# Optimization experiments

Hardware: AMD Instinct MI355X
Metric: run time of the kernel (lower is better)

## Reference

```python
import jax, jax.numpy as jnp
import numpy as np

N = 50000          # nodes
E = 1_600_000      # edges
IN_DIM = 64
HID = 64
HEADS = 2
EDGE_DIM = 8
OUT_DIM = 2
NEG_SLOPE = 0.2    # PyG GATConv default negative_slope


def _gat_params(key, in_ch, out_ch, heads, edge_dim, concat):
    ks = jax.random.split(key, 6)
    s = 0.1
    W = jax.random.normal(ks[0], (in_ch, heads * out_ch), jnp.float32) * s
    a_src = jax.random.normal(ks[1], (heads, out_ch), jnp.float32) * s
    a_dst = jax.random.normal(ks[2], (heads, out_ch), jnp.float32) * s
    We = jax.random.normal(ks[3], (edge_dim, heads * out_ch), jnp.float32) * s
    a_e = jax.random.normal(ks[4], (heads, out_ch), jnp.float32) * s
    b = jnp.zeros((heads * out_ch if concat else out_ch,), jnp.float32)
    return W, a_src, a_dst, We, a_e, b


def gat_conv(x, edge_index, edge_attr, W, a_src, a_dst, We, a_e, b, heads, out_ch, concat):
    # Faithful PyG GATConv with edge_dim, add_self_loops=True, fill_value='mean'.
    n = x.shape[0]
    src0, dst0 = edge_index[0], edge_index[1]
    # self-loop edge_attr = mean of incoming edge attrs (scatter-mean over dst)
    cnt = jax.ops.segment_sum(jnp.ones((src0.shape[0],), x.dtype), dst0, num_segments=n)
    loop_attr = jax.ops.segment_sum(edge_attr, dst0, num_segments=n) / jnp.maximum(cnt, 1.0)[:, None]
    loop = jnp.arange(n, dtype=src0.dtype)
    src = jnp.concatenate([src0, loop])
    dst = jnp.concatenate([dst0, loop])
    ea = jnp.concatenate([edge_attr, loop_attr], axis=0)          # [E+N, edge_dim]

    h = (x @ W).reshape(n, heads, out_ch)                          # [N, H, C]
    al_src = jnp.einsum('nhc,hc->nh', h, a_src)                    # [N, H]
    al_dst = jnp.einsum('nhc,hc->nh', h, a_dst)
    e = (ea @ We).reshape(-1, heads, out_ch)                       # [E+N, H, C]
    al_edge = jnp.einsum('ehc,hc->eh', e, a_e)

    alpha = jax.nn.leaky_relu(al_src[src] + al_dst[dst] + al_edge, NEG_SLOPE)  # [E+N, H]
    # segment softmax over destination node (every dst has a self loop)
    amax = jax.ops.segment_max(alpha, dst, num_segments=n)
    ex = jnp.exp(alpha - amax[dst])
    denom = jax.ops.segment_sum(ex, dst, num_segments=n)
    w = ex / (denom[dst] + 1e-16)

    out = jax.ops.segment_sum(h[src] * w[:, :, None], dst, num_segments=n)     # [N, H, C]
    out = out.reshape(n, heads * out_ch) if concat else out.mean(axis=1)
    return out + b


def setup_inputs() -> dict:
    key = jax.random.key(0)
    ks = jax.random.split(key, 8)
    inp = {
        'x': jax.random.normal(ks[0], (N, IN_DIM), jnp.float32),
        'edge_index': jax.random.randint(ks[1], (2, E), 0, N, dtype=jnp.int32),
        'edge_attr': jax.random.normal(ks[2], (E, EDGE_DIM), jnp.float32),
    }
    # layer 0: in -> hid, heads=1, concat=True
    for name, p in zip(['W0', 'as0', 'ad0', 'We0', 'ae0', 'b0'], _gat_params(ks[3], IN_DIM, HID, 1, EDGE_DIM, True)):
        inp[name] = p
    # layers 1,2: hid -> hid, heads=HEADS, concat=False
    for name, p in zip(['W1', 'as1', 'ad1', 'We1', 'ae1', 'b1'], _gat_params(ks[4], HID, HID, HEADS, EDGE_DIM, False)):
        inp[name] = p
    for name, p in zip(['W2', 'as2', 'ad2', 'We2', 'ae2', 'b2'], _gat_params(ks[5], HID, HID, HEADS, EDGE_DIM, False)):
        inp[name] = p
    # final: hid -> out_dim, heads=1, concat=True
    for name, p in zip(['W3', 'as3', 'ad3', 'We3', 'ae3', 'b3'], _gat_params(ks[6], HID, OUT_DIM, 1, EDGE_DIM, True)):
        inp[name] = p
    return inp


def reference(x, edge_index, edge_attr,
              W0, as0, ad0, We0, ae0, b0,
              W1, as1, ad1, We1, ae1, b1,
              W2, as2, ad2, We2, ae2, b2,
              W3, as3, ad3, We3, ae3, b3):
    h = jax.nn.relu(gat_conv(x, edge_index, edge_attr, W0, as0, ad0, We0, ae0, b0, 1, HID, True))
    h = jax.nn.relu(gat_conv(h, edge_index, edge_attr, W1, as1, ad1, We1, ae1, b1, HEADS, HID, False))
    h = jax.nn.relu(gat_conv(h, edge_index, edge_attr, W2, as2, ad2, We2, ae2, b2, HEADS, HID, False))
    return gat_conv(h, edge_index, edge_attr, W3, as3, ad3, We3, ae3, b3, 1, OUT_DIM, True)
```

## Files before the change

### kernel.cpp

```cpp
#include <hip/hip_runtime.h>
#include <math.h>


#define GSZ 256
#define CAPB 10240
#define CHUNK 4096
#define CAP_C 9984

__device__ __forceinline__ float wave_sum64(float v) {
#pragma unroll
  for (int o = 32; o >= 1; o >>= 1) v += __shfl_xor(v, o);
  return v;
}
__device__ __forceinline__ float dot8(const float4& a, const float4& b,
                                      const float* c) {
  return a.x * c[0] + a.y * c[1] + a.z * c[2] + a.w * c[3] + b.x * c[4] +
         b.y * c[5] + b.z * c[6] + b.w * c[7];
}


__global__ __launch_bounds__(256) void bin_kernel(const int* __restrict__ src,
                                                  const int* __restrict__ dst,
                                                  int* __restrict__ bfill,
                                                  int2* __restrict__ bbuf,
                                                  int E_) {
  __shared__ int histo[256];
  __shared__ int scanb[256];
  __shared__ int segstart[256];
  __shared__ int gbase[256];
  __shared__ int cur[256];
  __shared__ int2 stage[CHUNK];
  __shared__ int gtarg[CHUNK];
  const int t = threadIdx.x;
  const int e0 = blockIdx.x * CHUNK;
  const int cnt = min(CHUNK, E_ - e0);
  histo[t] = 0;
  __syncthreads();
  int myd[CHUNK / 256];
#pragma unroll
  for (int k = 0; k < CHUNK / 256; ++k) {
    int i = t + k * 256;
    int d = -1;
    if (i < cnt) {
      d = dst[e0 + i];
      atomicAdd(&histo[d >> 8], 1);
    }
    myd[k] = d;
  }
  __syncthreads();
  const int v = histo[t];
  int acc = v;
  scanb[t] = v;
  __syncthreads();
#pragma unroll
  for (int o = 1; o < 256; o <<= 1) {
    int u = (t >= o) ? scanb[t - o] : 0;
    __syncthreads();
    acc += u;
    scanb[t] = acc;
    __syncthreads();
  }
  int gp = 0;
  if (v > 0) gp = atomicAdd(&bfill[t], v);
  segstart[t] = acc - v;
  gbase[t] = t * CAPB + min(gp, CAPB - v);
  cur[t] = 0;
  __syncthreads();
#pragma unroll
  for (int k = 0; k < CHUNK / 256; ++k) {
    int i = t + k * 256;
    int d = myd[k];
    if (d >= 0) {
      int b = d >> 8;
      int s = src[e0 + i];
      int p = atomicAdd(&cur[b], 1);
      int sl = segstart[b] + p;
      stage[sl] = make_int2(s, (e0 + i) | ((d & 255) << 21));
      gtarg[sl] = gbase[b] + p;
    }
  }
  __syncthreads();
  for (int i = t; i < cnt; i += 256) bbuf[gtarg[i]] = stage[i];
}

__global__ __launch_bounds__(256) void count_kernel(
    const int* __restrict__ bfill, const int2* __restrict__ bbuf,
    int* __restrict__ cnt, int n) {
  __shared__ int h[256];
  const int b = blockIdx.x;
  const int t = threadIdx.x;
  h[t] = 0;
  __syncthreads();
  const int m = min(bfill[b], CAPB);
  const int2* reg = bbuf + (size_t)b * CAPB;
  for (int i = t; i < m; i += 256) {
    int dl = ((unsigned)reg[i].y) >> 21;
    atomicAdd(&h[dl], 1);
  }
  __syncthreads();
  int node = b * GSZ + t;
  if (node < n) cnt[node] = h[t];
}

__global__ __launch_bounds__(256) void scan1_kernel(const int* __restrict__ cnt,
                                                    int* __restrict__ rowp,
                                                    int* __restrict__ bsum,
                                                    int n) {
  __shared__ int sd[256];
  const int t = threadIdx.x;
  const int base = blockIdx.x * 1024 + t * 4;
  int v0 = (base + 0 < n) ? cnt[base + 0] + 1 : 0;
  int v1 = (base + 1 < n) ? cnt[base + 1] + 1 : 0;
  int v2 = (base + 2 < n) ? cnt[base + 2] + 1 : 0;
  int v3 = (base + 3 < n) ? cnt[base + 3] + 1 : 0;
  const int s = v0 + v1 + v2 + v3;
  sd[t] = s;
  __syncthreads();
  int acc = s;
#pragma unroll
  for (int o = 1; o < 256; o <<= 1) {
    int u = (t >= o) ? sd[t - o] : 0;
    __syncthreads();
    acc += u;
    sd[t] = acc;
    __syncthreads();
  }
  int excl = acc - s;
  if (base + 0 < n) rowp[base + 0] = excl;
  if (base + 1 < n) rowp[base + 1] = excl + v0;
  if (base + 2 < n) rowp[base + 2] = excl + v0 + v1;
  if (base + 3 < n) rowp[base + 3] = excl + v0 + v1 + v2;
  if (t == 255) bsum[blockIdx.x] = acc;
}

__global__ void scan2_kernel(int* __restrict__ bsum, int nb) {
  const int lane = threadIdx.x;
  int v = (lane < nb) ? bsum[lane] : 0;
  int incl = v;
#pragma unroll
  for (int o = 1; o < 64; o <<= 1) {
    int u = __shfl_up(incl, o);
    if (lane >= o) incl += u;
  }
  if (lane < nb) bsum[lane] = incl - v;
  if (lane == 63) bsum[nb] = incl;
}

__global__ void scan3_kernel(int* __restrict__ rowp,
                             const int* __restrict__ bsum, int n, int nb) {
  int i = blockIdx.x * 256 + threadIdx.x;
  if (i >= n) return;
  rowp[i] += bsum[i >> 10];
  if (i == 0) rowp[n] = bsum[nb];
}

__global__ __launch_bounds__(256) void place_kernel(
    const int* __restrict__ rowp, const int* __restrict__ bfill,
    const int2* __restrict__ bbuf, int* __restrict__ col_src,
    int* __restrict__ eidA, int n, int E_) {
  __shared__ int rp[GSZ + 1];
  __shared__ int cur[GSZ];
  __shared__ int2 stage[CAP_C];
  const int b = blockIdx.x;
  const int t = threadIdx.x;
  const int lo = b * GSZ;
  const int nk = min(GSZ, n - lo);
  for (int i = t; i <= nk; i += 256) rp[i] = rowp[lo + i];
  cur[t] = 0;
  __syncthreads();
  const int s0 = rp[0];
  const int span = rp[nk] - s0;
  const bool fits = (span <= CAP_C);
  const int m = min(bfill[b], CAPB);
  const int2* reg = bbuf + (size_t)b * CAPB;
  for (int i = t; i < m; i += 256) {
    int2 pl = reg[i];
    int dl = ((unsigned)pl.y) >> 21;
    int e2 = pl.y & 0x1FFFFF;
    int p = atomicAdd(&cur[dl], 1);
    int slot = rp[dl] + p;
    if (fits) stage[slot - s0] = make_int2(pl.x, e2);
    else { col_src[slot] = pl.x; eidA[slot] = e2; }
  }
  if (t < nk) {
    int slot = rp[t + 1] - 1;
    int node = lo + t;
    if (fits) stage[slot - s0] = make_int2(node, E_ + node);
    else { col_src[slot] = node; eidA[slot] = E_ + node; }
  }
  __syncthreads();
  if (fits) {
    for (int i = t; i < span; i += 256) {
      int2 v = stage[i];
      col_src[s0 + i] = v.x;
      eidA[s0 + i] = v.y;
    }
  }
}

__global__ void comb_all_kernel(const float* __restrict__ We0,
                                const float* __restrict__ ae0,
                                const float* __restrict__ We1,
                                const float* __restrict__ ae1,
                                const float* __restrict__ We2,
                                const float* __restrict__ ae2,
                                const float* __restrict__ We3,
                                const float* __restrict__ ae3,
                                float* __restrict__ comb) {
  int t = threadIdx.x;
  if (t >= 48) return;
  float s = 0.f;
  if (t < 8) {
    int d = t;
    for (int c = 0; c < 64; ++c) s += We0[d * 64 + c] * ae0[c];
  } else if (t < 24) {
    int idx = t - 8, h = idx >> 3, d = idx & 7;
    for (int c = 0; c < 64; ++c) s += We1[d * 128 + h * 64 + c] * ae1[h * 64 + c];
  } else if (t < 40) {
    int idx = t - 24, h = idx >> 3, d = idx & 7;
    for (int c = 0; c < 64; ++c) s += We2[d * 128 + h * 64 + c] * ae2[h * 64 + c];
  } else {
    int d = t - 40;
    for (int c = 0; c < 2; ++c) s += We3[d * 2 + c] * ae3[c];
  }
  comb[t] = s;
}

__global__ __launch_bounds__(256) void edge_prep_kernel(
    const int* __restrict__ row_ptr, const int* __restrict__ eid,
    const float* __restrict__ ea, const float* __restrict__ comb,
    float* __restrict__ edot0, float* __restrict__ edot1,
    float* __restrict__ edot2, float* __restrict__ edot3, int n, int E_) {
  __shared__ float cb[48];
  if (threadIdx.x < 48) cb[threadIdx.x] = comb[threadIdx.x];
  __syncthreads();
  const int lane = threadIdx.x & 63;
  const int node = blockIdx.x * 4 + (threadIdx.x >> 6);
  if (node >= n) return;

  const int start = row_ptr[node];
  const int selfpos = row_ptr[node + 1] - 1;

  float s0 = 0.f, s1 = 0.f, s2 = 0.f, s3 = 0.f, s4 = 0.f, s5 = 0.f, s6 = 0.f,
        s7 = 0.f;
  for (int i = start + lane; i < selfpos; i += 64) {
    int id = eid[i];
    const float4* v = reinterpret_cast<const float4*>(ea + (size_t)id * 8);
    float4 a = v[0], b = v[1];
    s0 += a.x; s1 += a.y; s2 += a.z; s3 += a.w;
    s4 += b.x; s5 += b.y; s6 += b.z; s7 += b.w;
    edot0[i] = dot8(a, b, cb + 0);
    edot1[2 * i + 0] = dot8(a, b, cb + 8);
    edot1[2 * i + 1] = dot8(a, b, cb + 16);
    edot2[2 * i + 0] = dot8(a, b, cb + 24);
    edot2[2 * i + 1] = dot8(a, b, cb + 32);
    edot3[i] = dot8(a, b, cb + 40);
  }
#pragma unroll
  for (int o = 32; o >= 1; o >>= 1) {
    s0 += __shfl_xor(s0, o); s1 += __shfl_xor(s1, o);
    s2 += __shfl_xor(s2, o); s3 += __shfl_xor(s3, o);
    s4 += __shfl_xor(s4, o); s5 += __shfl_xor(s5, o);
    s6 += __shfl_xor(s6, o); s7 += __shfl_xor(s7, o);
  }
  if (lane == 0) {
    float deg = (float)(selfpos - start);
    float inv = 1.f / fmaxf(deg, 1.f);
    float4 a = make_float4(s0 * inv, s1 * inv, s2 * inv, s3 * inv);
    float4 b = make_float4(s4 * inv, s5 * inv, s6 * inv, s7 * inv);
    int i = selfpos;
    edot0[i] = dot8(a, b, cb + 0);
    edot1[2 * i + 0] = dot8(a, b, cb + 8);
    edot1[2 * i + 1] = dot8(a, b, cb + 16);
    edot2[2 * i + 0] = dot8(a, b, cb + 24);
    edot2[2 * i + 1] = dot8(a, b, cb + 32);
    edot3[i] = dot8(a, b, cb + 40);
  }
}


template <int HC, int H>
__global__ __launch_bounds__(256) void gemm_proj_kernel(
    const float* __restrict__ x, const float* __restrict__ W,
    const float* __restrict__ a_src, const float* __restrict__ a_dst,
    float* __restrict__ h, float* __restrict__ al_src,
    float* __restrict__ al_dst, int n) {
  constexpr int IN = 64;
  constexpr int C = HC / H;
  __shared__ float xs[32][IN];
  const int tid = threadIdx.x;
  const int j = tid % HC;
  const int rsub = tid / HC;
  constexpr int RPP = 256 / HC > 0 ? 256 / HC : 1;

  float wr[IN];
#pragma unroll
  for (int k = 0; k < IN; ++k) wr[k] = W[k * HC + j];
  const float asj = a_src[j];
  const float adj = a_dst[j];

  const int row0 = blockIdx.x * 32;
  {
    const float4* xv = reinterpret_cast<const float4*>(x);
    float4* xsv = reinterpret_cast<float4*>(&xs[0][0]);
    for (int i = tid; i < 32 * IN / 4; i += 256) {
      int r = i / (IN / 4);
      int row = row0 + r;
      float4 v = make_float4(0.f, 0.f, 0.f, 0.f);
      if (row < n) v = xv[(size_t)row * (IN / 4) + (i % (IN / 4))];
      xsv[i] = v;
    }
  }
  __syncthreads();

  for (int rb = 0; rb < 32; rb += RPP) {
    int r = rb + rsub;
    if (r >= 32) break;
    int row = row0 + r;
    float acc = 0.f;
#pragma unroll
    for (int k4 = 0; k4 < IN / 4; ++k4) {
      float4 xv = *reinterpret_cast<const float4*>(&xs[r][k4 * 4]);
      acc += xv.x * wr[k4 * 4 + 0] + xv.y * wr[k4 * 4 + 1] +
             xv.z * wr[k4 * 4 + 2] + xv.w * wr[k4 * 4 + 3];
    }
    if (row < n) {
      size_t oidx = (H == 2)
                        ? ((size_t)(j >> 6) * ((size_t)n * 64) +
                           (size_t)row * 64 + (j & 63))
                        : ((size_t)row * HC + j);
      h[oidx] = acc;
    }
    float ps = acc * asj;
    float pd = acc * adj;
#pragma unroll
    for (int o = C / 2; o >= 1; o >>= 1) {
      ps += __shfl_xor(ps, o);
      pd += __shfl_xor(pd, o);
    }
    if (row < n && (j % C) == 0) {
      int hh = j / C;
      al_src[(size_t)row * H + hh] = ps;
      al_dst[(size_t)row * H + hh] = pd;
    }
  }
}

template <int C, bool RELU>
__global__ __launch_bounds__(256) void gat_node_kernel(
    const int* __restrict__ row_ptr, const int* __restrict__ col_src,
    const float* __restrict__ edot, const float* __restrict__ h_proj,
    const float* __restrict__ al_src, const float* __restrict__ al_dst,
    const float* __restrict__ bias, float* __restrict__ out, int n) {
  const int lane = threadIdx.x & 63;
  const int node = blockIdx.x * 4 + (threadIdx.x >> 6);
  if (node >= n) return;

  const float adn = al_dst[node];
  const int start = row_ptr[node];
  const int end = row_ptr[node + 1];

  float denp = 0.f;
  float4 acc4 = make_float4(0.f, 0.f, 0.f, 0.f);
  float accp = 0.f;

  const int sub = lane & 15;
  const int grp16 = lane >> 4;

  for (int base = start; base < end; base += 64) {
    const int i = base + lane;
    const bool valid = (i < end);
    int s = 0;
    float ex = 0.f;
    if (valid) {
      s = col_src[i];
      float a = al_src[s] + adn + edot[i];
      a = (a > 0.f) ? a : 0.2f * a;
      ex = __expf(a);
    }
    denp += ex;

    const int cntc = min(64, end - base);
    if (C == 2) {
      const int half = lane >> 1;
      const int ch = lane & 1;
#pragma unroll
      for (int sb = 0; sb < 2; ++sb) {
        int tt = sb * 32 + half;
        int sv = __shfl(s, tt);
        float w = __shfl(ex, tt);
        if (tt < cntc) accp += w * h_proj[sv * 2 + ch];
      }
    } else {
      const int nit = (cntc + 3) >> 2;
      for (int it0 = 0; it0 < nit; it0 += 4) {
        float4 v[4];
        float w[4];
#pragma unroll
        for (int u = 0; u < 4; ++u) {
          int tt = (it0 + u) * 4 + grp16;
          int sv = __shfl(s, tt);
          w[u] = __shfl(ex, tt);
          v[u] = *reinterpret_cast<const float4*>(h_proj + (size_t)sv * 64 +
                                                  sub * 4);
        }
#pragma unroll
        for (int u = 0; u < 4; ++u) {
          acc4.x += w[u] * v[u].x; acc4.y += w[u] * v[u].y;
          acc4.z += w[u] * v[u].z; acc4.w += w[u] * v[u].w;
        }
      }
    }
  }

  const float den = wave_sum64(denp);

  if (C == 2) {
#pragma unroll
    for (int o = 2; o <= 32; o <<= 1) accp += __shfl_xor(accp, o);
    if (lane < 2) {
      float v = accp / (den + 1e-16f) + bias[lane];
      if (RELU) v = fmaxf(v, 0.f);
      out[node * 2 + lane] = v;
    }
  } else {
    acc4.x += __shfl_xor(acc4.x, 16); acc4.x += __shfl_xor(acc4.x, 32);
    acc4.y += __shfl_xor(acc4.y, 16); acc4.y += __shfl_xor(acc4.y, 32);
    acc4.z += __shfl_xor(acc4.z, 16); acc4.z += __shfl_xor(acc4.z, 32);
    acc4.w += __shfl_xor(acc4.w, 16); acc4.w += __shfl_xor(acc4.w, 32);
    if (lane < 16) {
      float inv = 1.f / (den + 1e-16f);
      float4 bv = *reinterpret_cast<const float4*>(bias + sub * 4);
      float4 o;
      o.x = acc4.x * inv + bv.x; o.y = acc4.y * inv + bv.y;
      o.z = acc4.z * inv + bv.z; o.w = acc4.w * inv + bv.w;
      if (RELU) {
        o.x = fmaxf(o.x, 0.f); o.y = fmaxf(o.y, 0.f);
        o.z = fmaxf(o.z, 0.f); o.w = fmaxf(o.w, 0.f);
      }
      *reinterpret_cast<float4*>(out + (size_t)node * 64 + sub * 4) = o;
    }
  }
}

template <bool FIRST>
__global__ __launch_bounds__(256) void gat_head_kernel(
    const int* __restrict__ row_ptr, const int* __restrict__ col_src,
    const float* __restrict__ edot2, int head,
    const float* __restrict__ hplane, const float* __restrict__ al_src2,
    const float* __restrict__ al_dst2, const float* __restrict__ bias,
    float* __restrict__ partial, float* __restrict__ out, int n) {
  const int lane = threadIdx.x & 63;
  const int node = blockIdx.x * 4 + (threadIdx.x >> 6);
  if (node >= n) return;

  const float adn = al_dst2[node * 2 + head];
  const int start = row_ptr[node];
  const int end = row_ptr[node + 1];

  float denp = 0.f;
  float4 acc4 = make_float4(0.f, 0.f, 0.f, 0.f);

  const int sub = lane & 15;
  const int grp16 = lane >> 4;

  for (int base = start; base < end; base += 64) {
    const int i = base + lane;
    const bool valid = (i < end);
    int s = 0;
    float ex = 0.f;
    if (valid) {
      s = col_src[i];
      float a = al_src2[s * 2 + head] + adn + edot2[(size_t)i * 2 + head];
      a = (a > 0.f) ? a : 0.2f * a;
      ex = __expf(a);
    }
    denp += ex;

    const int cntc = min(64, end - base);
    const int nit = (cntc + 3) >> 2;
    for (int it0 = 0; it0 < nit; it0 += 4) {
      float4 v[4];
      float w[4];
#pragma unroll
      for (int u = 0; u < 4; ++u) {
        int tt = (it0 + u) * 4 + grp16;
        int sv = __shfl(s, tt);
        w[u] = __shfl(ex, tt);
        v[u] = *reinterpret_cast<const float4*>(hplane + (size_t)sv * 64 +
                                                sub * 4);
      }
#pragma unroll
      for (int u = 0; u < 4; ++u) {
        acc4.x += w[u] * v[u].x; acc4.y += w[u] * v[u].y;
        acc4.z += w[u] * v[u].z; acc4.w += w[u] * v[u].w;
      }
    }
  }

  const float den = wave_sum64(denp);

  acc4.x += __shfl_xor(acc4.x, 16); acc4.x += __shfl_xor(acc4.x, 32);
  acc4.y += __shfl_xor(acc4.y, 16); acc4.y += __shfl_xor(acc4.y, 32);
  acc4.z += __shfl_xor(acc4.z, 16); acc4.z += __shfl_xor(acc4.z, 32);
  acc4.w += __shfl_xor(acc4.w, 16); acc4.w += __shfl_xor(acc4.w, 32);
  if (lane < 16) {
    float inv = 1.f / (den + 1e-16f);
    if (FIRST) {
      float4 o;
      o.x = acc4.x * inv; o.y = acc4.y * inv;
      o.z = acc4.z * inv; o.w = acc4.w * inv;
      *reinterpret_cast<float4*>(partial + (size_t)node * 64 + sub * 4) = o;
    } else {
      float4 p =
          *reinterpret_cast<const float4*>(partial + (size_t)node * 64 + sub * 4);
      float4 bv = *reinterpret_cast<const float4*>(bias + sub * 4);
      float4 o;
      o.x = fmaxf((p.x + acc4.x * inv) * 0.5f + bv.x, 0.f);
      o.y = fmaxf((p.y + acc4.y * inv) * 0.5f + bv.y, 0.f);
      o.z = fmaxf((p.z + acc4.z * inv) * 0.5f + bv.z, 0.f);
      o.w = fmaxf((p.w + acc4.w * inv) * 0.5f + bv.w, 0.f);
      *reinterpret_cast<float4*>(out + (size_t)node * 64 + sub * 4) = o;
    }
  }
}


static inline size_t align_up(size_t v, size_t a) { return (v + a - 1) & ~(a - 1); }

extern "C" void kernel_launch(void* const* d_in, const int* in_sizes, int n_in,
                              void* d_out, int out_size, void* d_ws,
                              size_t ws_size, hipStream_t stream) {
  const float* x = (const float*)d_in[0];
  const int* ei = (const int*)d_in[1];
  const float* ea = (const float*)d_in[2];

  const int N = in_sizes[0] / 64;
  const int E = in_sizes[1] / 2;
  const int* src0 = ei;
  const int* dst0 = ei + E;
  const int M = E + N;

  const float* W[4] = {(const float*)d_in[3], (const float*)d_in[9],
                       (const float*)d_in[15], (const float*)d_in[21]};
  const float* As[4] = {(const float*)d_in[4], (const float*)d_in[10],
                        (const float*)d_in[16], (const float*)d_in[22]};
  const float* Ad[4] = {(const float*)d_in[5], (const float*)d_in[11],
                        (const float*)d_in[17], (const float*)d_in[23]};
  const float* We[4] = {(const float*)d_in[6], (const float*)d_in[12],
                        (const float*)d_in[18], (const float*)d_in[24]};
  const float* Ae[4] = {(const float*)d_in[7], (const float*)d_in[13],
                        (const float*)d_in[19], (const float*)d_in[25]};
  const float* B[4] = {(const float*)d_in[8], (const float*)d_in[14],
                       (const float*)d_in[20], (const float*)d_in[26]};

  char* p = (char*)d_ws;
  size_t off = 0;
  auto carve = [&](size_t bytes) {
    void* r = p + off;
    off = align_up(off + bytes, 256);
    return r;
  };
  const int NBK = (N + GSZ - 1) / GSZ;
  int* cnt = (int*)carve((size_t)N * 4);
  int* row_ptr = (int*)carve((size_t)(N + 1) * 4);
  int* bsum = (int*)carve((size_t)256 * 4);
  int* bfill = (int*)carve((size_t)NBK * 4);
  int2* bbuf = (int2*)carve((size_t)NBK * CAPB * 8);
  int* col_src = (int*)carve((size_t)M * 4);
  int* eid = (int*)carve((size_t)M * 4);
  float* comb = (float*)carve(256);
  float* edot0 = (float*)carve((size_t)M * 4);
  float* edot1 = (float*)carve((size_t)M * 8);
  float* edot2 = (float*)carve((size_t)M * 8);
  float* edot3 = (float*)carve((size_t)M * 4);
  float* al_src = (float*)carve((size_t)N * 2 * 4);
  float* al_dst = (float*)carve((size_t)N * 2 * 4);
  float* h_proj = (float*)carve((size_t)N * 128 * 4);
  float* buf_a = (float*)carve((size_t)N * 64 * 4);
  float* buf_b = (float*)carve((size_t)N * 64 * 4);
  float* partial = (float*)bbuf;
  (void)ws_size;

  const int nb = (N + 1023) / 1024;

  hipMemsetAsync(bfill, 0, (size_t)NBK * 4, stream);
  bin_kernel<<<(E + CHUNK - 1) / CHUNK, 256, 0, stream>>>(src0, dst0, bfill,
                                                          bbuf, E);
  count_kernel<<<NBK, 256, 0, stream>>>(bfill, bbuf, cnt, N);
  scan1_kernel<<<nb, 256, 0, stream>>>(cnt, row_ptr, bsum, N);
  scan2_kernel<<<1, 64, 0, stream>>>(bsum, nb);
  scan3_kernel<<<(N + 255) / 256, 256, 0, stream>>>(row_ptr, bsum, N, nb);
  place_kernel<<<NBK, 256, 0, stream>>>(row_ptr, bfill, bbuf, col_src, eid, N,
                                        E);
  comb_all_kernel<<<1, 64, 0, stream>>>(We[0], Ae[0], We[1], Ae[1], We[2],
                                        Ae[2], We[3], Ae[3], comb);
  edge_prep_kernel<<<(N + 3) / 4, 256, 0, stream>>>(
      row_ptr, eid, ea, comb, edot0, edot1, edot2, edot3, N, E);

  const int gemm_grid = (N + 31) / 32;
  const int node_grid = (N + 3) / 4;
  const size_t plane = (size_t)N * 64;

  gemm_proj_kernel<64, 1><<<gemm_grid, 256, 0, stream>>>(
      x, W[0], As[0], Ad[0], h_proj, al_src, al_dst, N);
  gat_node_kernel<64, true><<<node_grid, 256, 0, stream>>>(
      row_ptr, col_src, edot0, h_proj, al_src, al_dst, B[0], buf_a, N);

  gemm_proj_kernel<128, 2><<<gemm_grid, 256, 0, stream>>>(
      buf_a, W[1], As[1], Ad[1], h_proj, al_src, al_dst, N);
  gat_head_kernel<true><<<node_grid, 256, 0, stream>>>(
      row_ptr, col_src, edot1, 0, h_proj, al_src, al_dst, B[1], partial,
      nullptr, N);
  gat_head_kernel<false><<<node_grid, 256, 0, stream>>>(
      row_ptr, col_src, edot1, 1, h_proj + plane, al_src, al_dst, B[1],
      partial, buf_b, N);

  gemm_proj_kernel<128, 2><<<gemm_grid, 256, 0, stream>>>(
      buf_b, W[2], As[2], Ad[2], h_proj, al_src, al_dst, N);
  gat_head_kernel<true><<<node_grid, 256, 0, stream>>>(
      row_ptr, col_src, edot2, 0, h_proj, al_src, al_dst, B[2], partial,
      nullptr, N);
  gat_head_kernel<false><<<node_grid, 256, 0, stream>>>(
      row_ptr, col_src, edot2, 1, h_proj + plane, al_src, al_dst, B[2],
      partial, buf_a, N);

  gemm_proj_kernel<2, 1><<<gemm_grid, 256, 0, stream>>>(
      buf_a, W[3], As[3], Ad[3], h_proj, al_src, al_dst, N);
  gat_node_kernel<2, false><<<node_grid, 256, 0, stream>>>(
      row_ptr, col_src, edot3, h_proj, al_src, al_dst, B[3], (float*)d_out, N);
}
```

Measured before the change: 479.8 us.

## Split per-head edge/attention arrays into planar layout and double-buffer gather loads

Stores per-head edge logits and per-node attention scalars as separate contiguous planes instead of interleaved pairs, so each per-head aggregation pass reads only the data it needs with unit stride. It also rewrites the neighbor gather loop in the node and head kernels into a two-buffer software pipeline that issues the next batch of feature loads before doing the FMAs on the current one. This costs more registers per thread, which may lower occupancy.

```diff
diff --git a/kernel.cpp b/kernel.cpp
--- a/kernel.cpp
+++ b/kernel.cpp
@@ -229,8 +229,9 @@
 __global__ __launch_bounds__(256) void edge_prep_kernel(
     const int* __restrict__ row_ptr, const int* __restrict__ eid,
     const float* __restrict__ ea, const float* __restrict__ comb,
-    float* __restrict__ edot0, float* __restrict__ edot1,
-    float* __restrict__ edot2, float* __restrict__ edot3, int n, int E_) {
+    float* __restrict__ edot0, float* __restrict__ e1a,
+    float* __restrict__ e1b, float* __restrict__ e2a,
+    float* __restrict__ e2b, float* __restrict__ edot3, int n, int E_) {
   __shared__ float cb[48];
   if (threadIdx.x < 48) cb[threadIdx.x] = comb[threadIdx.x];
   __syncthreads();
@@ -250,10 +251,10 @@
     s0 += a.x; s1 += a.y; s2 += a.z; s3 += a.w;
     s4 += b.x; s5 += b.y; s6 += b.z; s7 += b.w;
     edot0[i] = dot8(a, b, cb + 0);
-    edot1[2 * i + 0] = dot8(a, b, cb + 8);
-    edot1[2 * i + 1] = dot8(a, b, cb + 16);
-    edot2[2 * i + 0] = dot8(a, b, cb + 24);
-    edot2[2 * i + 1] = dot8(a, b, cb + 32);
+    e1a[i] = dot8(a, b, cb + 8);
+    e1b[i] = dot8(a, b, cb + 16);
+    e2a[i] = dot8(a, b, cb + 24);
+    e2b[i] = dot8(a, b, cb + 32);
     edot3[i] = dot8(a, b, cb + 40);
   }
 #pragma unroll
@@ -270,14 +271,13 @@
     float4 b = make_float4(s4 * inv, s5 * inv, s6 * inv, s7 * inv);
     int i = selfpos;
     edot0[i] = dot8(a, b, cb + 0);
-    edot1[2 * i + 0] = dot8(a, b, cb + 8);
-    edot1[2 * i + 1] = dot8(a, b, cb + 16);
-    edot2[2 * i + 0] = dot8(a, b, cb + 24);
-    edot2[2 * i + 1] = dot8(a, b, cb + 32);
+    e1a[i] = dot8(a, b, cb + 8);
+    e1b[i] = dot8(a, b, cb + 16);
+    e2a[i] = dot8(a, b, cb + 24);
+    e2b[i] = dot8(a, b, cb + 32);
     edot3[i] = dot8(a, b, cb + 40);
   }
 }
-
 
 template <int HC, int H>
 __global__ __launch_bounds__(256) void gemm_proj_kernel(
@@ -340,8 +340,8 @@
     }
     if (row < n && (j % C) == 0) {
       int hh = j / C;
-      al_src[(size_t)row * H + hh] = ps;
-      al_dst[(size_t)row * H + hh] = pd;
+      al_src[(size_t)hh * n + row] = ps;
+      al_dst[(size_t)hh * n + row] = pd;
     }
   }
 }
@@ -392,23 +392,35 @@
         if (tt < cntc) accp += w * h_proj[sv * 2 + ch];
       }
     } else {
-      const int nit = (cntc + 3) >> 2;
-      for (int it0 = 0; it0 < nit; it0 += 4) {
-        float4 v[4];
-        float w[4];
+      auto issue = [&](int g, float4 (&v)[4], float (&w)[4]) {
 #pragma unroll
         for (int u = 0; u < 4; ++u) {
-          int tt = (it0 + u) * 4 + grp16;
+          int tt = (g * 4 + u) * 4 + grp16;
           int sv = __shfl(s, tt);
           w[u] = __shfl(ex, tt);
           v[u] = *reinterpret_cast<const float4*>(h_proj + (size_t)sv * 64 +
                                                   sub * 4);
         }
+      };
+      auto fma4 = [&](float4 (&v)[4], float (&w)[4]) {
 #pragma unroll
         for (int u = 0; u < 4; ++u) {
           acc4.x += w[u] * v[u].x; acc4.y += w[u] * v[u].y;
           acc4.z += w[u] * v[u].z; acc4.w += w[u] * v[u].w;
         }
+      };
+      const int nbat = (cntc + 15) >> 4;
+      float4 va[4], vb[4];
+      float wa[4], wb[4];
+      issue(0, va, wa);
+      int g = 0;
+      for (;;) {
+        if (g + 1 < nbat) issue(g + 1, vb, wb);
+        fma4(va, wa);
+        if (++g >= nbat) break;
+        if (g + 1 < nbat) issue(g + 1, va, wa);
+        fma4(vb, wb);
+        if (++g >= nbat) break;
       }
     }
   }
@@ -446,15 +458,15 @@
 template <bool FIRST>
 __global__ __launch_bounds__(256) void gat_head_kernel(
     const int* __restrict__ row_ptr, const int* __restrict__ col_src,
-    const float* __restrict__ edot2, int head,
-    const float* __restrict__ hplane, const float* __restrict__ al_src2,
-    const float* __restrict__ al_dst2, const float* __restrict__ bias,
-    float* __restrict__ partial, float* __restrict__ out, int n) {
+    const float* __restrict__ edotH, const float* __restrict__ hplane,
+    const float* __restrict__ al_srcH, const float* __restrict__ al_dstH,
+    const float* __restrict__ bias, float* __restrict__ partial,
+    float* __restrict__ out, int n) {
   const int lane = threadIdx.x & 63;
   const int node = blockIdx.x * 4 + (threadIdx.x >> 6);
   if (node >= n) return;
 
-  const float adn = al_dst2[node * 2 + head];
+  const float adn = al_dstH[node];
   const int start = row_ptr[node];
   const int end = row_ptr[node + 1];
 
@@ -471,30 +483,42 @@
     float ex = 0.f;
     if (valid) {
       s = col_src[i];
-      float a = al_src2[s * 2 + head] + adn + edot2[(size_t)i * 2 + head];
+      float a = al_srcH[s] + adn + edotH[i];
       a = (a > 0.f) ? a : 0.2f * a;
       ex = __expf(a);
     }
     denp += ex;
 
     const int cntc = min(64, end - base);
-    const int nit = (cntc + 3) >> 2;
-    for (int it0 = 0; it0 < nit; it0 += 4) {
-      float4 v[4];
-      float w[4];
+    auto issue = [&](int g, float4 (&v)[4], float (&w)[4]) {
 #pragma unroll
       for (int u = 0; u < 4; ++u) {
-        int tt = (it0 + u) * 4 + grp16;
+        int tt = (g * 4 + u) * 4 + grp16;
         int sv = __shfl(s, tt);
         w[u] = __shfl(ex, tt);
         v[u] = *reinterpret_cast<const float4*>(hplane + (size_t)sv * 64 +
                                                 sub * 4);
       }
+    };
+    auto fma4 = [&](float4 (&v)[4], float (&w)[4]) {
 #pragma unroll
       for (int u = 0; u < 4; ++u) {
         acc4.x += w[u] * v[u].x; acc4.y += w[u] * v[u].y;
         acc4.z += w[u] * v[u].z; acc4.w += w[u] * v[u].w;
       }
+    };
+    const int nbat = (cntc + 15) >> 4;
+    float4 va[4], vb[4];
+    float wa[4], wb[4];
+    issue(0, va, wa);
+    int g = 0;
+    for (;;) {
+      if (g + 1 < nbat) issue(g + 1, vb, wb);
+      fma4(va, wa);
+      if (++g >= nbat) break;
+      if (g + 1 < nbat) issue(g + 1, va, wa);
+      fma4(vb, wb);
+      if (++g >= nbat) break;
     }
   }
 
@@ -571,8 +595,10 @@
   int* eid = (int*)carve((size_t)M * 4);
   float* comb = (float*)carve(256);
   float* edot0 = (float*)carve((size_t)M * 4);
-  float* edot1 = (float*)carve((size_t)M * 8);
-  float* edot2 = (float*)carve((size_t)M * 8);
+  float* e1a = (float*)carve((size_t)M * 4);
+  float* e1b = (float*)carve((size_t)M * 4);
+  float* e2a = (float*)carve((size_t)M * 4);
+  float* e2b = (float*)carve((size_t)M * 4);
   float* edot3 = (float*)carve((size_t)M * 4);
   float* al_src = (float*)carve((size_t)N * 2 * 4);
   float* al_dst = (float*)carve((size_t)N * 2 * 4);
@@ -596,7 +622,7 @@
   comb_all_kernel<<<1, 64, 0, stream>>>(We[0], Ae[0], We[1], Ae[1], We[2],
                                         Ae[2], We[3], Ae[3], comb);
   edge_prep_kernel<<<(N + 3) / 4, 256, 0, stream>>>(
-      row_ptr, eid, ea, comb, edot0, edot1, edot2, edot3, N, E);
+      row_ptr, eid, ea, comb, edot0, e1a, e1b, e2a, e2b, edot3, N, E);
 
   const int gemm_grid = (N + 31) / 32;
   const int node_grid = (N + 3) / 4;
@@ -610,19 +636,17 @@
   gemm_proj_kernel<128, 2><<<gemm_grid, 256, 0, stream>>>(
       buf_a, W[1], As[1], Ad[1], h_proj, al_src, al_dst, N);
   gat_head_kernel<true><<<node_grid, 256, 0, stream>>>(
-      row_ptr, col_src, edot1, 0, h_proj, al_src, al_dst, B[1], partial,
-      nullptr, N);
+      row_ptr, col_src, e1a, h_proj, al_src, al_dst, B[1], partial, nullptr, N);
   gat_head_kernel<false><<<node_grid, 256, 0, stream>>>(
-      row_ptr, col_src, edot1, 1, h_proj + plane, al_src, al_dst, B[1],
+      row_ptr, col_src, e1b, h_proj + plane, al_src + N, al_dst + N, B[1],
       partial, buf_b, N);
 
   gemm_proj_kernel<128, 2><<<gemm_grid, 256, 0, stream>>>(
       buf_b, W[2], As[2], Ad[2], h_proj, al_src, al_dst, N);
   gat_head_kernel<true><<<node_grid, 256, 0, stream>>>(
-      row_ptr, col_src, edot2, 0, h_proj, al_src, al_dst, B[2], partial,
-      nullptr, N);
+      row_ptr, col_src, e2a, h_proj, al_src, al_dst, B[2], partial, nullptr, N);
   gat_head_kernel<false><<<node_grid, 256, 0, stream>>>(
-      row_ptr, col_src, edot2, 1, h_proj + plane, al_src, al_dst, B[2],
+      row_ptr, col_src, e2b, h_proj + plane, al_src + N, al_dst + N, B[2],
       partial, buf_a, N);
 
   gemm_proj_kernel<2, 1><<<gemm_grid, 256, 0, stream>>>(
```

Measured after the change: 475.5 us, median of 2. No clear change (-0.9%).
